# Kernel optimization log

Hardware: AMD Instinct MI355X
Metric: run time of the kernel (lower is better)

Reference implementation:

```python
import jax, jax.numpy as jnp
import numpy as np

B, S, D, H = 2, 2048, 1024, 16
DH = D // H  # dim per head (dim_singl_head)
SCALE = 0.02


def layer_norm(x, g, b, eps=1e-5):
    m = jnp.mean(x, axis=-1, keepdims=True)
    v = jnp.mean((x - m) ** 2, axis=-1, keepdims=True)
    return (x - m) / jnp.sqrt(v + eps) * g + b


def setup_inputs() -> dict:
    key = jax.random.key(0)
    ks = jax.random.split(key, 12)
    return {
        "query": jax.random.normal(ks[0], (B, S, D), jnp.float32),
        "key": jax.random.normal(ks[1], (B, S, D), jnp.float32),
        "value": jax.random.normal(ks[2], (B, S, D), jnp.float32),
        "mask": jax.random.randint(ks[3], (B, S), 0, 2).astype(jnp.int32),
        "Wq": jax.random.normal(ks[4], (D, D), jnp.float32) * SCALE,
        "bq": jnp.zeros((D,), jnp.float32),
        "Wk": jax.random.normal(ks[5], (D, D), jnp.float32) * SCALE,
        "bk": jnp.zeros((D,), jnp.float32),
        "Wv": jax.random.normal(ks[6], (D, D), jnp.float32) * SCALE,
        "bv": jnp.zeros((D,), jnp.float32),
        "g_att": jnp.ones((DH,), jnp.float32),
        "b_att": jnp.zeros((DH,), jnp.float32),
        "Wres": jax.random.normal(ks[7], (D, D), jnp.float32) * SCALE,
        "bres": jnp.zeros((D,), jnp.float32),
        "g_out": jnp.ones((D,), jnp.float32),
        "b_out": jnp.zeros((D,), jnp.float32),
    }


def reference(query, key, value, mask, Wq, bq, Wk, bk, Wv, bv,
              g_att, b_att, Wres, bres, g_out, b_out):
    # split heads: torch's split(dh,-1)+cat(dim=0) == [H,B,S,dh] layout
    def heads(x):
        return x.reshape(B, S, H, DH).transpose(2, 0, 1, 3)  # [H,B,S,dh]

    q = heads(query @ Wq + bq)
    k = heads(key @ Wk + bk)
    v = heads(value @ Wv + bv)

    # additive mask: (1-mask)*-1e9, broadcast [1,B,1,Sk]
    madd = (1.0 - mask.astype(q.dtype))[None, :, None, :] * -1e9

    scores = jnp.einsum('hbqd,hbkd->hbqk', q, k) / np.float32(np.sqrt(DH))
    w = jax.nn.softmax(scores + madd, axis=-1)
    out = jnp.einsum('hbqk,hbkd->hbqd', w, v)

    out = out + q                         # residual_att
    out = layer_norm(out, g_att, b_att)   # per-head LayerNorm on dh

    # concat heads back: [H,B,S,dh] -> [B,S,H*dh]
    out = out.transpose(1, 2, 0, 3).reshape(B, S, D)

    out = out + jnp.tanh(out @ Wres + bres)  # residual_out branch
    out = layer_norm(out, g_out, b_out)      # norm_out
    return jnp.tanh(out)                     # final activation
```

## Files before the change

kernel.cpp:

```cpp
#include <hip/hip_runtime.h>
#include <cstdint>
#include <cstddef>

#define BB 2
#define SS 2048
#define DD 1024
#define HH 16
#define DHH 64
#define MROWS (BB*SS)

typedef short short8 __attribute__((ext_vector_type(8)));
typedef short short4v __attribute__((ext_vector_type(4)));
typedef float floatx4 __attribute__((ext_vector_type(4)));

#define GAS __attribute__((address_space(1)))
#define LAS __attribute__((address_space(3)))

#if !defined(__HIP_DEVICE_COMPILE__)
#define MFMA16(a, b, c) (c)
#elif __has_builtin(__builtin_amdgcn_mfma_f32_16x16x16bf16_1k)
#define MFMA16(a, b, c) __builtin_amdgcn_mfma_f32_16x16x16bf16_1k((a), (b), (c), 0, 0, 0)
#elif __has_builtin(__builtin_amdgcn_mfma_f32_16x16x16_bf16)
#define MFMA16(a, b, c) __builtin_amdgcn_mfma_f32_16x16x16_bf16((a), (b), (c), 0, 0, 0)
#elif __has_builtin(__builtin_amdgcn_mfma_f32_16x16x16_bf16_1k)
#define MFMA16(a, b, c) __builtin_amdgcn_mfma_f32_16x16x16_bf16_1k((a), (b), (c), 0, 0, 0)
#else
#error "no 16x16x16 bf16 MFMA builtin found on device pass"
#endif

__device__ __forceinline__ float4 ld4(const float* p) { return *(const float4*)p; }

__device__ __forceinline__ short f2bf(float x) {
    unsigned u = __builtin_bit_cast(unsigned, x);
    unsigned r = (u + 0x7fffu + ((u >> 16) & 1u)) >> 16;
    return (short)r;
}

__device__ __forceinline__ void gl_lds16(const short* g, short* l) {
    __builtin_amdgcn_global_load_lds((const GAS unsigned int*)g,
                                     (LAS unsigned int*)l, 16, 0, 0);
}

__global__ __launch_bounds__(256) void transpose_w_kernel(
    const float* __restrict__ W0, const float* __restrict__ W1,
    const float* __restrict__ W2, const float* __restrict__ W3,
    short* __restrict__ T0, short* __restrict__ T1,
    short* __restrict__ T2, short* __restrict__ T3)
{
    const float* W; short* T;
    if (blockIdx.z == 0)      { W = W0; T = T0; }
    else if (blockIdx.z == 1) { W = W1; T = T1; }
    else if (blockIdx.z == 2) { W = W2; T = T2; }
    else                      { W = W3; T = T3; }

    __shared__ short tile[64 * 72];
    const int t  = threadIdx.x;
    const int k0 = blockIdx.x * 64, n0 = blockIdx.y * 64;
#pragma unroll
    for (int i = 0; i < 4; i++) {
        int flat = i * 256 + t;
        int row = flat >> 4;
        int c4  = (flat & 15) * 4;
        float4 v = ld4(W + (size_t)(k0 + row) * DD + n0 + c4);
        tile[(c4 + 0) * 72 + row] = f2bf(v.x);
        tile[(c4 + 1) * 72 + row] = f2bf(v.y);
        tile[(c4 + 2) * 72 + row] = f2bf(v.z);
        tile[(c4 + 3) * 72 + row] = f2bf(v.w);
    }
    __syncthreads();
#pragma unroll
    for (int i = 0; i < 4; i++) {
        int flat = i * 256 + t;
        int nrow = flat >> 4;
        int kc   = (flat & 15) * 4;
        short4v pk = *(short4v*)&tile[nrow * 72 + kc];
        *(short4v*)(T + (size_t)(n0 + nrow) * DD + k0 + kc) = pk;
    }
}

__global__ __launch_bounds__(256) void gemm_bf16_kernel(
    const float* __restrict__ A0, const float* __restrict__ A1, const float* __restrict__ A2,
    const short* __restrict__ Bt0, const short* __restrict__ Bt1, const short* __restrict__ Bt2,
    const float* __restrict__ b0, const float* __restrict__ b1, const float* __restrict__ b2,
    float* __restrict__ Cf0, float* __restrict__ Cf1, float* __restrict__ Cf2,
    short* __restrict__ Cb0, short* __restrict__ Cb1, short* __restrict__ Cb2,
    short* __restrict__ Ct0, short* __restrict__ Ct1, short* __restrict__ Ct2,
    float cs0, float cs1, float cs2)
{
    const float* A; const short* Bt; const float* bias;
    float* Cf; short* Cb; short* Ct; float cbs;
    if (blockIdx.z == 0)      { A = A0; Bt = Bt0; bias = b0; Cf = Cf0; Cb = Cb0; Ct = Ct0; cbs = cs0; }
    else if (blockIdx.z == 1) { A = A1; Bt = Bt1; bias = b1; Cf = Cf1; Cb = Cb1; Ct = Ct1; cbs = cs1; }
    else                      { A = A2; Bt = Bt2; bias = b2; Cf = Cf2; Cb = Cb2; Ct = Ct2; cbs = cs2; }

    __shared__ __align__(16) short As[2 * 128 * 32];
    __shared__ __align__(16) short Bs[2 * 128 * 32];

    const int tid  = threadIdx.x;
    const int lane = tid & 63;
    const int wave = tid >> 6;
    const int quad = lane >> 4;
    const int l15  = lane & 15;
    const int m0 = blockIdx.y * 128;
    const int n0 = blockIdx.x * 128;
    const int wr = (wave >> 1) * 64;
    const int wc = (wave & 1) * 64;

    const int arow = tid >> 2;
    const int ach  = tid & 3;

    floatx4 acc[4][4];
#pragma unroll
    for (int mt = 0; mt < 4; mt++)
#pragma unroll
        for (int nt = 0; nt < 4; nt++) acc[mt][nt] = (floatx4)0.0f;

    float4 fa[2][2];
#pragma unroll
    for (int i = 0; i < 2; i++) {
        int c = tid + i * 256;
        gl_lds16(Bt + (size_t)(n0 + (c >> 2)) * DD + (c & 3) * 8, &Bs[c * 8]);
    }
#pragma unroll
    for (int i = 0; i < 2; i++) {
        const float* ap = A + (size_t)(m0 + arow + i * 64) * DD + ach * 8;
        fa[i][0] = ld4(ap);
        fa[i][1] = ld4(ap + 4);
    }

    for (int kk = 0; kk < 32; kk++) {
        const int bufo = (kk & 1) * 4096;
#pragma unroll
        for (int i = 0; i < 2; i++) {
            short8 s8;
            s8[0] = f2bf(fa[i][0].x); s8[1] = f2bf(fa[i][0].y);
            s8[2] = f2bf(fa[i][0].z); s8[3] = f2bf(fa[i][0].w);
            s8[4] = f2bf(fa[i][1].x); s8[5] = f2bf(fa[i][1].y);
            s8[6] = f2bf(fa[i][1].z); s8[7] = f2bf(fa[i][1].w);
            *(short8*)&As[bufo + (arow + i * 64) * 32 + ach * 8] = s8;
        }
        __syncthreads();

        if (kk < 31) {
            const int k0n = (kk + 1) * 32;
            const int nbuf = bufo ^ 4096;
#pragma unroll
            for (int i = 0; i < 2; i++) {
                int c = tid + i * 256;
                gl_lds16(Bt + (size_t)(n0 + (c >> 2)) * DD + k0n + (c & 3) * 8,
                         &Bs[nbuf + c * 8]);
            }
#pragma unroll
            for (int i = 0; i < 2; i++) {
                const float* ap = A + (size_t)(m0 + arow + i * 64) * DD + k0n + ach * 8;
                fa[i][0] = ld4(ap);
                fa[i][1] = ld4(ap + 4);
            }
        }

        short8 af[4], bf[4];
#pragma unroll
        for (int mt = 0; mt < 4; mt++)
            af[mt] = *(const short8*)&As[bufo + (wr + mt * 16 + l15) * 32 + quad * 8];
#pragma unroll
        for (int nt = 0; nt < 4; nt++)
            bf[nt] = *(const short8*)&Bs[bufo + (wc + nt * 16 + l15) * 32 + quad * 8];
#pragma unroll
        for (int mt = 0; mt < 4; mt++)
#pragma unroll
            for (int nt = 0; nt < 4; nt++)
                acc[mt][nt] = __builtin_amdgcn_mfma_f32_16x16x32_bf16(af[mt], bf[nt], acc[mt][nt], 0, 0, 0);
    }

    float biasv[4];
#pragma unroll
    for (int nt = 0; nt < 4; nt++) biasv[nt] = bias[n0 + wc + nt * 16 + l15];

    if (Cf || Cb) {
#pragma unroll
        for (int mt = 0; mt < 4; mt++)
#pragma unroll
            for (int r = 0; r < 4; r++) {
                const int m = m0 + wr + mt * 16 + quad * 4 + r;
                const size_t rowb = (size_t)m * DD + n0 + wc;
#pragma unroll
                for (int nt = 0; nt < 4; nt++) {
                    float v = acc[mt][nt][r] + biasv[nt];
                    if (Cf) Cf[rowb + nt * 16 + l15] = v;
                    if (Cb) Cb[rowb + nt * 16 + l15] = f2bf(v * cbs);
                }
            }
    }
    if (Ct) {
#pragma unroll
        for (int mt = 0; mt < 4; mt++) {
            const int mbase = m0 + wr + mt * 16 + quad * 4;
            const int bb = mbase >> 11;
            const int s0 = mbase & 2047;
#pragma unroll
            for (int nt = 0; nt < 4; nt++) {
                const int c = n0 + wc + nt * 16 + l15;
                short4v pk;
#pragma unroll
                for (int r = 0; r < 4; r++) pk[r] = f2bf(acc[mt][nt][r] + biasv[nt]);
                *(short4v*)(Ct + ((size_t)(bb * 1024 + c)) * SS + s0) = pk;
            }
        }
    }
}

__global__ __launch_bounds__(256, 4) void attn_mfma_kernel(
    const short* __restrict__ Qb, const short* __restrict__ Kb, const short* __restrict__ Vt,
    const float* __restrict__ Qf, const int* __restrict__ mask,
    const float* __restrict__ g_att, const float* __restrict__ b_att,
    float* __restrict__ X)
{
    const int tid  = threadIdx.x;
    const int lane = tid & 63;
    const int wave = tid >> 6;
    const int quad = lane >> 4;
    const int l15  = lane & 15;

    const int h  = blockIdx.y;
    const int b  = blockIdx.z;
    const int q0 = blockIdx.x * 128;
    const int bS = b * SS;

    __shared__ __align__(16) short Ks[2 * 64 * 72];
    __shared__ __align__(16) short Vs[2 * 64 * 72];
    __shared__ __align__(16) float smv[2 * 64];

    short8 qf[2][2];
#pragma unroll
    for (int qt = 0; qt < 2; qt++)
#pragma unroll
        for (int s = 0; s < 2; s++)
            qf[qt][s] = *(const short8*)(Qb +
                (size_t)(bS + q0 + wave * 32 + qt * 16 + l15) * DD + h * 64 + s * 32 + quad * 8);

    floatx4 o[4][2];
#pragma unroll
    for (int dt = 0; dt < 4; dt++)
#pragma unroll
        for (int qt = 0; qt < 2; qt++) o[dt][qt] = (floatx4)0.0f;
    float lsum[2] = {0.0f, 0.0f};

    const int srow = tid >> 3;
    const int sch  = tid & 7;

    short8 kreg[2], vreg[2];
    float mreg;
#pragma unroll
    for (int i = 0; i < 2; i++) {
        int row = srow + i * 32;
        kreg[i] = *(const short8*)(Kb + (size_t)(bS + row) * DD + h * 64 + sch * 8);
        vreg[i] = *(const short8*)(Vt + (size_t)(b * 1024 + h * 64 + row) * SS + sch * 8);
    }
    mreg = (tid < 64) ? (float)mask[bS + tid] : 0.0f;

    for (int kt = 0; kt < SS / 64; kt++) {
        const int bufo = (kt & 1) * (64 * 72);
        const int mvo  = (kt & 1) * 64;
#pragma unroll
        for (int i = 0; i < 2; i++) {
            int row = srow + i * 32;
            *(short8*)&Ks[bufo + row * 72 + sch * 8] = kreg[i];
            *(short8*)&Vs[bufo + row * 72 + sch * 8] = vreg[i];
        }
        if (tid < 64) smv[mvo + tid] = mreg;

        if (kt < SS / 64 - 1) {
            const int k0n = (kt + 1) * 64;
#pragma unroll
            for (int i = 0; i < 2; i++) {
                int row = srow + i * 32;
                kreg[i] = *(const short8*)(Kb + (size_t)(bS + k0n + row) * DD + h * 64 + sch * 8);
                vreg[i] = *(const short8*)(Vt + (size_t)(b * 1024 + h * 64 + row) * SS + k0n + sch * 8);
            }
            mreg = (tid < 64) ? (float)mask[bS + k0n + tid] : 0.0f;
        }

        __builtin_amdgcn_s_waitcnt(0xC07F);
        __builtin_amdgcn_s_barrier();

        short4v pf[4][2];
#pragma unroll
        for (int kt4 = 0; kt4 < 4; kt4++) {
            short8 kf0 = *(const short8*)&Ks[bufo + (kt4 * 16 + l15) * 72 + quad * 8];
            short8 kf1 = *(const short8*)&Ks[bufo + (kt4 * 16 + l15) * 72 + 32 + quad * 8];
            floatx4 mv = *(const floatx4*)&smv[mvo + kt4 * 16 + quad * 4];
#pragma unroll
            for (int qt = 0; qt < 2; qt++) {
                floatx4 st = (floatx4)0.0f;
                st = __builtin_amdgcn_mfma_f32_16x16x32_bf16(kf0, qf[qt][0], st, 0, 0, 0);
                st = __builtin_amdgcn_mfma_f32_16x16x32_bf16(kf1, qf[qt][1], st, 0, 0, 0);
                short4v pk;
#pragma unroll
                for (int r = 0; r < 4; r++) {
                    float p = __expf(st[r]) * mv[r];
                    lsum[qt] += p;
                    pk[r] = f2bf(p);
                }
                pf[kt4][qt] = pk;
            }
        }

#pragma unroll
        for (int dt = 0; dt < 4; dt++)
#pragma unroll
            for (int ks = 0; ks < 4; ks++) {
                short4v vf = *(const short4v*)&Vs[bufo + (dt * 16 + l15) * 72 + ks * 16 + quad * 4];
#pragma unroll
                for (int qt = 0; qt < 2; qt++)
                    o[dt][qt] = MFMA16(vf, pf[ks][qt], o[dt][qt]);
            }
    }

#pragma unroll
    for (int qt = 0; qt < 2; qt++) {
        lsum[qt] += __shfl_xor(lsum[qt], 16);
        lsum[qt] += __shfl_xor(lsum[qt], 32);
    }

#pragma unroll
    for (int qt = 0; qt < 2; qt++) {
        const int q = q0 + wave * 32 + qt * 16 + l15;
        const size_t base = (size_t)(bS + q) * DD + h * 64;
        const float rl = 1.0f / lsum[qt];

        float x[4][4];
        float sum = 0.0f;
#pragma unroll
        for (int dt = 0; dt < 4; dt++) {
            float4 qr = ld4(Qf + base + dt * 16 + quad * 4);
            x[dt][0] = o[dt][qt][0] * rl + qr.x;
            x[dt][1] = o[dt][qt][1] * rl + qr.y;
            x[dt][2] = o[dt][qt][2] * rl + qr.z;
            x[dt][3] = o[dt][qt][3] * rl + qr.w;
            sum += x[dt][0] + x[dt][1] + x[dt][2] + x[dt][3];
        }
        sum += __shfl_xor(sum, 16);
        sum += __shfl_xor(sum, 32);
        const float mu = sum * (1.0f / 64.0f);

        float vs = 0.0f;
#pragma unroll
        for (int dt = 0; dt < 4; dt++)
#pragma unroll
            for (int r = 0; r < 4; r++) { float d = x[dt][r] - mu; vs += d * d; }
        vs += __shfl_xor(vs, 16);
        vs += __shfl_xor(vs, 32);
        const float rstd = rsqrtf(vs * (1.0f / 64.0f) + 1e-5f);

#pragma unroll
        for (int dt = 0; dt < 4; dt++) {
            float4 gv = ld4(g_att + dt * 16 + quad * 4);
            float4 bv = ld4(b_att + dt * 16 + quad * 4);
            float4 y;
            y.x = (x[dt][0] - mu) * rstd * gv.x + bv.x;
            y.y = (x[dt][1] - mu) * rstd * gv.y + bv.y;
            y.z = (x[dt][2] - mu) * rstd * gv.z + bv.z;
            y.w = (x[dt][3] - mu) * rstd * gv.w + bv.w;
            *(float4*)(X + base + dt * 16 + quad * 4) = y;
        }
    }
}

__global__ __launch_bounds__(256) void lnout_kernel(
    const float* __restrict__ X, const float* __restrict__ Y,
    const float* __restrict__ g, const float* __restrict__ bcoef,
    float* __restrict__ out)
{
    const int r = blockIdx.x;
    const int t = threadIdx.x;
    const size_t base = (size_t)r * DD + (t << 2);
    float4 x = ld4(X + base);
    float4 y = ld4(Y + base);
    float4 z;
    z.x = x.x + tanhf(y.x);
    z.y = x.y + tanhf(y.y);
    z.z = x.z + tanhf(y.z);
    z.w = x.w + tanhf(y.w);

    __shared__ float red[4];
    __shared__ float stats[2];
    const int w = t >> 6;

    float sv = z.x + z.y + z.z + z.w;
#pragma unroll
    for (int off = 32; off > 0; off >>= 1) sv += __shfl_down(sv, off);
    if ((t & 63) == 0) red[w] = sv;
    __syncthreads();
    if (t == 0) stats[0] = (red[0] + red[1] + red[2] + red[3]) * (1.0f / 1024.0f);
    __syncthreads();
    const float mu = stats[0];

    float4 d;
    d.x = z.x - mu; d.y = z.y - mu; d.z = z.z - mu; d.w = z.w - mu;
    float s2 = d.x * d.x + d.y * d.y + d.z * d.z + d.w * d.w;
#pragma unroll
    for (int off = 32; off > 0; off >>= 1) s2 += __shfl_down(s2, off);
    if ((t & 63) == 0) red[w] = s2;
    __syncthreads();
    if (t == 0) stats[1] = rsqrtf((red[0] + red[1] + red[2] + red[3]) * (1.0f / 1024.0f) + 1e-5f);
    __syncthreads();
    const float rstd = stats[1];

    float4 gv = ld4(g + (t << 2));
    float4 bv = ld4(bcoef + (t << 2));
    float4 o;
    o.x = tanhf(d.x * rstd * gv.x + bv.x);
    o.y = tanhf(d.y * rstd * gv.y + bv.y);
    o.z = tanhf(d.z * rstd * gv.z + bv.z);
    o.w = tanhf(d.w * rstd * gv.w + bv.w);
    *(float4*)(out + base) = o;
}

extern "C" void kernel_launch(void* const* d_in, const int* in_sizes, int n_in,
                              void* d_out, int out_size, void* d_ws, size_t ws_size,
                              hipStream_t stream)
{
    const float* query = (const float*)d_in[0];
    const float* key   = (const float*)d_in[1];
    const float* value = (const float*)d_in[2];
    const int*   mask  = (const int*)  d_in[3];
    const float* Wq    = (const float*)d_in[4];
    const float* bq    = (const float*)d_in[5];
    const float* Wk    = (const float*)d_in[6];
    const float* bk    = (const float*)d_in[7];
    const float* Wv    = (const float*)d_in[8];
    const float* bv    = (const float*)d_in[9];
    const float* g_att = (const float*)d_in[10];
    const float* b_att = (const float*)d_in[11];
    const float* Wres  = (const float*)d_in[12];
    const float* bres  = (const float*)d_in[13];
    const float* g_out = (const float*)d_in[14];
    const float* b_out = (const float*)d_in[15];

    const size_t MAT = (size_t)MROWS * DD;
    float* fws = (float*)d_ws;
    float* Qw = fws;
    float* Xw = fws + MAT;
    float* Yw = fws + 2 * MAT;
    short* Qb = (short*)(fws + 3 * MAT);
    short* Kb = Qb + MAT;
    short* Vt = Kb + MAT;
    short* Wtq = Vt + MAT;
    short* Wtk = Wtq + DD * DD;
    short* Wtv = Wtk + DD * DD;
    short* Wtr = Wtv + DD * DD;

    transpose_w_kernel<<<dim3(16, 16, 4), 256, 0, stream>>>(
        Wq, Wk, Wv, Wres, Wtq, Wtk, Wtv, Wtr);

    gemm_bf16_kernel<<<dim3(8, 32, 3), 256, 0, stream>>>(
        query, key, value, Wtq, Wtk, Wtv, bq, bk, bv,
        Qw, nullptr, nullptr,
        Qb, Kb, nullptr,
        nullptr, nullptr, Vt,
        0.125f, 1.0f, 1.0f);

    attn_mfma_kernel<<<dim3(SS / 128, HH, BB), 256, 0, stream>>>(
        Qb, Kb, Vt, Qw, mask, g_att, b_att, Xw);

    gemm_bf16_kernel<<<dim3(8, 32, 1), 256, 0, stream>>>(
        Xw, Xw, Xw, Wtr, Wtr, Wtr, bres, bres, bres,
        Yw, Yw, Yw, nullptr, nullptr, nullptr, nullptr, nullptr, nullptr,
        1.0f, 1.0f, 1.0f);

    lnout_kernel<<<MROWS, 256, 0, stream>>>(Xw, Yw, g_out, b_out, (float*)d_out);
}
```

Measured before the change: 309.9 us.

## Pre-convert activations to bf16, restructure GEMM loads and attention tiling

```diff
diff --git a/kernel.cpp b/kernel.cpp
--- a/kernel.cpp
+++ b/kernel.cpp
@@ -16,18 +16,6 @@
 #define GAS __attribute__((address_space(1)))
 #define LAS __attribute__((address_space(3)))
 
-#if !defined(__HIP_DEVICE_COMPILE__)
-#define MFMA16(a, b, c) (c)
-#elif __has_builtin(__builtin_amdgcn_mfma_f32_16x16x16bf16_1k)
-#define MFMA16(a, b, c) __builtin_amdgcn_mfma_f32_16x16x16bf16_1k((a), (b), (c), 0, 0, 0)
-#elif __has_builtin(__builtin_amdgcn_mfma_f32_16x16x16_bf16)
-#define MFMA16(a, b, c) __builtin_amdgcn_mfma_f32_16x16x16_bf16((a), (b), (c), 0, 0, 0)
-#elif __has_builtin(__builtin_amdgcn_mfma_f32_16x16x16_bf16_1k)
-#define MFMA16(a, b, c) __builtin_amdgcn_mfma_f32_16x16x16_bf16_1k((a), (b), (c), 0, 0, 0)
-#else
-#error "no 16x16x16 bf16 MFMA builtin found on device pass"
-#endif
-
 __device__ __forceinline__ float4 ld4(const float* p) { return *(const float4*)p; }
 
 __device__ __forceinline__ short f2bf(float x) {
@@ -39,6 +27,23 @@
 __device__ __forceinline__ void gl_lds16(const short* g, short* l) {
     __builtin_amdgcn_global_load_lds((const GAS unsigned int*)g,
                                      (LAS unsigned int*)l, 16, 0, 0);
+}
+
+__global__ __launch_bounds__(256) void convert_kernel(
+    const float* __restrict__ s0, const float* __restrict__ s1, const float* __restrict__ s2,
+    short* __restrict__ d0, short* __restrict__ d1, short* __restrict__ d2)
+{
+    const float* s; short* d;
+    if (blockIdx.z == 0)      { s = s0; d = d0; }
+    else if (blockIdx.z == 1) { s = s1; d = d1; }
+    else                      { s = s2; d = d2; }
+    size_t idx = ((size_t)blockIdx.x * 256 + threadIdx.x) * 8;
+    float4 a = ld4(s + idx);
+    float4 b = ld4(s + idx + 4);
+    short8 p;
+    p[0] = f2bf(a.x); p[1] = f2bf(a.y); p[2] = f2bf(a.z); p[3] = f2bf(a.w);
+    p[4] = f2bf(b.x); p[5] = f2bf(b.y); p[6] = f2bf(b.z); p[7] = f2bf(b.w);
+    *(short8*)(d + idx) = p;
 }
 
 __global__ __launch_bounds__(256) void transpose_w_kernel(
@@ -78,23 +83,51 @@
     }
 }
 
+__global__ __launch_bounds__(256) void transpose_v_kernel(
+    const short* __restrict__ Vb, short* __restrict__ Vt)
+{
+    __shared__ short tile[64 * 72];
+    const int t  = threadIdx.x;
+    const int sb = blockIdx.x * 64;
+    const int cb = blockIdx.y * 64;
+    const int b  = sb >> 11;
+    const int s0 = sb & 2047;
+#pragma unroll
+    for (int i = 0; i < 2; i++) {
+        int flat = i * 256 + t;
+        int r  = flat >> 3;
+        int ch = flat & 7;
+        short8 v = *(const short8*)(Vb + (size_t)(sb + r) * DD + cb + ch * 8);
+#pragma unroll
+        for (int j = 0; j < 8; j++) tile[(ch * 8 + j) * 72 + r] = v[j];
+    }
+    __syncthreads();
+#pragma unroll
+    for (int i = 0; i < 2; i++) {
+        int flat = i * 256 + t;
+        int cr = flat >> 3;
+        int sc = flat & 7;
+        short8 w = *(const short8*)&tile[cr * 72 + sc * 8];
+        *(short8*)(Vt + ((size_t)(b * 1024 + cb + cr)) * SS + s0 + sc * 8) = w;
+    }
+}
+
 __global__ __launch_bounds__(256) void gemm_bf16_kernel(
-    const float* __restrict__ A0, const float* __restrict__ A1, const float* __restrict__ A2,
+    const short* __restrict__ A0, const short* __restrict__ A1, const short* __restrict__ A2,
     const short* __restrict__ Bt0, const short* __restrict__ Bt1, const short* __restrict__ Bt2,
     const float* __restrict__ b0, const float* __restrict__ b1, const float* __restrict__ b2,
     float* __restrict__ Cf0, float* __restrict__ Cf1, float* __restrict__ Cf2,
     short* __restrict__ Cb0, short* __restrict__ Cb1, short* __restrict__ Cb2,
-    short* __restrict__ Ct0, short* __restrict__ Ct1, short* __restrict__ Ct2,
     float cs0, float cs1, float cs2)
 {
-    const float* A; const short* Bt; const float* bias;
-    float* Cf; short* Cb; short* Ct; float cbs;
-    if (blockIdx.z == 0)      { A = A0; Bt = Bt0; bias = b0; Cf = Cf0; Cb = Cb0; Ct = Ct0; cbs = cs0; }
-    else if (blockIdx.z == 1) { A = A1; Bt = Bt1; bias = b1; Cf = Cf1; Cb = Cb1; Ct = Ct1; cbs = cs1; }
-    else                      { A = A2; Bt = Bt2; bias = b2; Cf = Cf2; Cb = Cb2; Ct = Ct2; cbs = cs2; }
-
-    __shared__ __align__(16) short As[2 * 128 * 32];
-    __shared__ __align__(16) short Bs[2 * 128 * 32];
+    const short* A; const short* Bt; const float* bias;
+    float* Cf; short* Cb; float cbs;
+    if (blockIdx.z == 0)      { A = A0; Bt = Bt0; bias = b0; Cf = Cf0; Cb = Cb0; cbs = cs0; }
+    else if (blockIdx.z == 1) { A = A1; Bt = Bt1; bias = b1; Cf = Cf1; Cb = Cb1; cbs = cs1; }
+    else                      { A = A2; Bt = Bt2; bias = b2; Cf = Cf2; Cb = Cb2; cbs = cs2; }
+
+    __shared__ __align__(16) short As[128 * 32];
+    __shared__ __align__(16) short Bs[128 * 32];
 
     const int tid  = threadIdx.x;
     const int lane = tid & 63;
@@ -106,65 +139,31 @@
     const int wr = (wave >> 1) * 64;
     const int wc = (wave & 1) * 64;
 
-    const int arow = tid >> 2;
-    const int ach  = tid & 3;
-
     floatx4 acc[4][4];
 #pragma unroll
     for (int mt = 0; mt < 4; mt++)
 #pragma unroll
         for (int nt = 0; nt < 4; nt++) acc[mt][nt] = (floatx4)0.0f;
 
-    float4 fa[2][2];
-#pragma unroll
-    for (int i = 0; i < 2; i++) {
-        int c = tid + i * 256;
-        gl_lds16(Bt + (size_t)(n0 + (c >> 2)) * DD + (c & 3) * 8, &Bs[c * 8]);
-    }
-#pragma unroll
-    for (int i = 0; i < 2; i++) {
-        const float* ap = A + (size_t)(m0 + arow + i * 64) * DD + ach * 8;
-        fa[i][0] = ld4(ap);
-        fa[i][1] = ld4(ap + 4);
-    }
-
-    for (int kk = 0; kk < 32; kk++) {
-        const int bufo = (kk & 1) * 4096;
-#pragma unroll
-        for (int i = 0; i < 2; i++) {
-            short8 s8;
-            s8[0] = f2bf(fa[i][0].x); s8[1] = f2bf(fa[i][0].y);
-            s8[2] = f2bf(fa[i][0].z); s8[3] = f2bf(fa[i][0].w);
-            s8[4] = f2bf(fa[i][1].x); s8[5] = f2bf(fa[i][1].y);
-            s8[6] = f2bf(fa[i][1].z); s8[7] = f2bf(fa[i][1].w);
-            *(short8*)&As[bufo + (arow + i * 64) * 32 + ach * 8] = s8;
-        }
+    for (int k0 = 0; k0 < DD; k0 += 32) {
         __syncthreads();
-
-        if (kk < 31) {
-            const int k0n = (kk + 1) * 32;
-            const int nbuf = bufo ^ 4096;
-#pragma unroll
-            for (int i = 0; i < 2; i++) {
-                int c = tid + i * 256;
-                gl_lds16(Bt + (size_t)(n0 + (c >> 2)) * DD + k0n + (c & 3) * 8,
-                         &Bs[nbuf + c * 8]);
-            }
-#pragma unroll
-            for (int i = 0; i < 2; i++) {
-                const float* ap = A + (size_t)(m0 + arow + i * 64) * DD + k0n + ach * 8;
-                fa[i][0] = ld4(ap);
-                fa[i][1] = ld4(ap + 4);
-            }
-        }
+#pragma unroll
+        for (int j = 0; j < 2; j++) {
+            int chunk = j * 256 + tid;
+            int row = chunk >> 2;
+            int ch  = chunk & 3;
+            gl_lds16(A  + (size_t)(m0 + row) * DD + k0 + ch * 8, &As[chunk * 8]);
+            gl_lds16(Bt + (size_t)(n0 + row) * DD + k0 + ch * 8, &Bs[chunk * 8]);
+        }
+        __syncthreads();
 
         short8 af[4], bf[4];
 #pragma unroll
         for (int mt = 0; mt < 4; mt++)
-            af[mt] = *(const short8*)&As[bufo + (wr + mt * 16 + l15) * 32 + quad * 8];
+            af[mt] = *(const short8*)&As[(wr + mt * 16 + l15) * 32 + quad * 8];
 #pragma unroll
         for (int nt = 0; nt < 4; nt++)
-            bf[nt] = *(const short8*)&Bs[bufo + (wc + nt * 16 + l15) * 32 + quad * 8];
+            bf[nt] = *(const short8*)&Bs[(wc + nt * 16 + l15) * 32 + quad * 8];
 #pragma unroll
         for (int mt = 0; mt < 4; mt++)
 #pragma unroll
@@ -176,44 +175,26 @@
 #pragma unroll
     for (int nt = 0; nt < 4; nt++) biasv[nt] = bias[n0 + wc + nt * 16 + l15];
 
-    if (Cf || Cb) {
-#pragma unroll
-        for (int mt = 0; mt < 4; mt++)
-#pragma unroll
-            for (int r = 0; r < 4; r++) {
-                const int m = m0 + wr + mt * 16 + quad * 4 + r;
-                const size_t rowb = (size_t)m * DD + n0 + wc;
-#pragma unroll
-                for (int nt = 0; nt < 4; nt++) {
-                    float v = acc[mt][nt][r] + biasv[nt];
-                    if (Cf) Cf[rowb + nt * 16 + l15] = v;
-                    if (Cb) Cb[rowb + nt * 16 + l15] = f2bf(v * cbs);
-                }
+#pragma unroll
+    for (int mt = 0; mt < 4; mt++)
+#pragma unroll
+        for (int r = 0; r < 4; r++) {
+            const int m = m0 + wr + mt * 16 + quad * 4 + r;
+            const size_t rowb = (size_t)m * DD + n0 + wc;
+#pragma unroll
+            for (int nt = 0; nt < 4; nt++) {
+                float v = acc[mt][nt][r] + biasv[nt];
+                if (Cf) Cf[rowb + nt * 16 + l15] = v;
+                if (Cb) Cb[rowb + nt * 16 + l15] = f2bf(v * cbs);
             }
-    }
-    if (Ct) {
-#pragma unroll
-        for (int mt = 0; mt < 4; mt++) {
-            const int mbase = m0 + wr + mt * 16 + quad * 4;
-            const int bb = mbase >> 11;
-            const int s0 = mbase & 2047;
-#pragma unroll
-            for (int nt = 0; nt < 4; nt++) {
-                const int c = n0 + wc + nt * 16 + l15;
-                short4v pk;
-#pragma unroll
-                for (int r = 0; r < 4; r++) pk[r] = f2bf(acc[mt][nt][r] + biasv[nt]);
-                *(short4v*)(Ct + ((size_t)(bb * 1024 + c)) * SS + s0) = pk;
-            }
-        }
-    }
-}
-
-__global__ __launch_bounds__(256, 4) void attn_mfma_kernel(
+        }
+}
+
+__global__ __launch_bounds__(256, 2) void attn_mfma_kernel(
     const short* __restrict__ Qb, const short* __restrict__ Kb, const short* __restrict__ Vt,
     const float* __restrict__ Qf, const int* __restrict__ mask,
     const float* __restrict__ g_att, const float* __restrict__ b_att,
-    float* __restrict__ X)
+    float* __restrict__ X, short* __restrict__ Xb)
 {
     const int tid  = threadIdx.x;
     const int lane = tid & 63;
@@ -223,27 +204,31 @@
 
     const int h  = blockIdx.y;
     const int b  = blockIdx.z;
-    const int q0 = blockIdx.x * 128;
+    const int q0 = blockIdx.x * 256;
+    const int qw0 = q0 + wave * 64;
     const int bS = b * SS;
 
     __shared__ __align__(16) short Ks[2 * 64 * 72];
     __shared__ __align__(16) short Vs[2 * 64 * 72];
+    __shared__ __align__(16) short Ps[4 * 64 * 72];
     __shared__ __align__(16) float smv[2 * 64];
 
-    short8 qf[2][2];
-#pragma unroll
-    for (int qt = 0; qt < 2; qt++)
+    short* Pw = &Ps[wave * 64 * 72];
+
+    short8 qf[4][2];
+#pragma unroll
+    for (int qt = 0; qt < 4; qt++)
 #pragma unroll
         for (int s = 0; s < 2; s++)
             qf[qt][s] = *(const short8*)(Qb +
-                (size_t)(bS + q0 + wave * 32 + qt * 16 + l15) * DD + h * 64 + s * 32 + quad * 8);
-
-    floatx4 o[4][2];
+                (size_t)(bS + qw0 + qt * 16 + l15) * DD + h * 64 + s * 32 + quad * 8);
+
+    floatx4 o[4][4];
 #pragma unroll
     for (int dt = 0; dt < 4; dt++)
 #pragma unroll
-        for (int qt = 0; qt < 2; qt++) o[dt][qt] = (floatx4)0.0f;
-    float lsum[2] = {0.0f, 0.0f};
+        for (int qt = 0; qt < 4; qt++) o[dt][qt] = (floatx4)0.0f;
+    float lsum[4] = {0.0f, 0.0f, 0.0f, 0.0f};
 
     const int srow = tid >> 3;
     const int sch  = tid & 7;
@@ -283,14 +268,13 @@
         __builtin_amdgcn_s_waitcnt(0xC07F);
         __builtin_amdgcn_s_barrier();
 
-        short4v pf[4][2];
 #pragma unroll
         for (int kt4 = 0; kt4 < 4; kt4++) {
             short8 kf0 = *(const short8*)&Ks[bufo + (kt4 * 16 + l15) * 72 + quad * 8];
             short8 kf1 = *(const short8*)&Ks[bufo + (kt4 * 16 + l15) * 72 + 32 + quad * 8];
             floatx4 mv = *(const floatx4*)&smv[mvo + kt4 * 16 + quad * 4];
 #pragma unroll
-            for (int qt = 0; qt < 2; qt++) {
+            for (int qt = 0; qt < 4; qt++) {
                 floatx4 st = (floatx4)0.0f;
                 st = __builtin_amdgcn_mfma_f32_16x16x32_bf16(kf0, qf[qt][0], st, 0, 0, 0);
                 st = __builtin_amdgcn_mfma_f32_16x16x32_bf16(kf1, qf[qt][1], st, 0, 0, 0);
@@ -301,30 +285,35 @@
                     lsum[qt] += p;
                     pk[r] = f2bf(p);
                 }
-                pf[kt4][qt] = pk;
+                *(short4v*)&Pw[(qt * 16 + l15) * 72 + kt4 * 16 + quad * 4] = pk;
             }
         }
 
 #pragma unroll
-        for (int dt = 0; dt < 4; dt++)
-#pragma unroll
-            for (int ks = 0; ks < 4; ks++) {
-                short4v vf = *(const short4v*)&Vs[bufo + (dt * 16 + l15) * 72 + ks * 16 + quad * 4];
-#pragma unroll
-                for (int qt = 0; qt < 2; qt++)
-                    o[dt][qt] = MFMA16(vf, pf[ks][qt], o[dt][qt]);
+        for (int s = 0; s < 2; s++) {
+            short8 pb[4];
+#pragma unroll
+            for (int qt = 0; qt < 4; qt++)
+                pb[qt] = *(const short8*)&Pw[(qt * 16 + l15) * 72 + s * 32 + quad * 8];
+#pragma unroll
+            for (int dt = 0; dt < 4; dt++) {
+                short8 vf = *(const short8*)&Vs[bufo + (dt * 16 + l15) * 72 + s * 32 + quad * 8];
+#pragma unroll
+                for (int qt = 0; qt < 4; qt++)
+                    o[dt][qt] = __builtin_amdgcn_mfma_f32_16x16x32_bf16(vf, pb[qt], o[dt][qt], 0, 0, 0);
             }
-    }
-
-#pragma unroll
-    for (int qt = 0; qt < 2; qt++) {
+        }
+    }
+
+#pragma unroll
+    for (int qt = 0; qt < 4; qt++) {
         lsum[qt] += __shfl_xor(lsum[qt], 16);
         lsum[qt] += __shfl_xor(lsum[qt], 32);
     }
 
 #pragma unroll
-    for (int qt = 0; qt < 2; qt++) {
-        const int q = q0 + wave * 32 + qt * 16 + l15;
+    for (int qt = 0; qt < 4; qt++) {
+        const int q = qw0 + qt * 16 + l15;
         const size_t base = (size_t)(bS + q) * DD + h * 64;
         const float rl = 1.0f / lsum[qt];
 
@@ -362,6 +351,9 @@
             y.z = (x[dt][2] - mu) * rstd * gv.z + bv.z;
             y.w = (x[dt][3] - mu) * rstd * gv.w + bv.w;
             *(float4*)(X + base + dt * 16 + quad * 4) = y;
+            short4v yb;
+            yb[0] = f2bf(y.x); yb[1] = f2bf(y.y); yb[2] = f2bf(y.z); yb[3] = f2bf(y.w);
+            *(short4v*)(Xb + base + dt * 16 + quad * 4) = yb;
         }
     }
 }
@@ -441,31 +433,40 @@
     float* fws = (float*)d_ws;
     float* Qw = fws;
     float* Xw = fws + MAT;
-    float* Yw = fws + 2 * MAT;
-    short* Qb = (short*)(fws + 3 * MAT);
-    short* Kb = Qb + MAT;
-    short* Vt = Kb + MAT;
-    short* Wtq = Vt + MAT;
+    short* Qb  = (short*)(fws + 2 * MAT);
+    short* Kb  = Qb + MAT;
+    short* Vt  = Kb + MAT;
+    short* qbf = Vt + MAT;
+    short* kbf = qbf + MAT;
+    short* vbf = kbf + MAT;
+    short* Wtq = vbf + MAT;
     short* Wtk = Wtq + DD * DD;
     short* Wtv = Wtk + DD * DD;
     short* Wtr = Wtv + DD * DD;
+    short* Vb = (short*)Xw;
+    short* Xb = qbf;
+    float* Yw = (float*)kbf;
+
+    convert_kernel<<<dim3(MAT / 2048, 1, 3), 256, 0, stream>>>(
+        query, key, value, qbf, kbf, vbf);
 
     transpose_w_kernel<<<dim3(16, 16, 4), 256, 0, stream>>>(
         Wq, Wk, Wv, Wres, Wtq, Wtk, Wtv, Wtr);
 
     gemm_bf16_kernel<<<dim3(8, 32, 3), 256, 0, stream>>>(
-        query, key, value, Wtq, Wtk, Wtv, bq, bk, bv,
+        qbf, kbf, vbf, Wtq, Wtk, Wtv, bq, bk, bv,
         Qw, nullptr, nullptr,
-        Qb, Kb, nullptr,
-        nullptr, nullptr, Vt,
+        Qb, Kb, Vb,
         0.125f, 1.0f, 1.0f);
 
-    attn_mfma_kernel<<<dim3(SS / 128, HH, BB), 256, 0, stream>>>(
-        Qb, Kb, Vt, Qw, mask, g_att, b_att, Xw);
+    transpose_v_kernel<<<dim3(64, 16), 256, 0, stream>>>(Vb, Vt);
+
+    attn_mfma_kernel<<<dim3(SS / 256, HH, BB), 256, 0, stream>>>(
+        Qb, Kb, Vt, Qw, mask, g_att, b_att, Xw, Xb);
 
     gemm_bf16_kernel<<<dim3(8, 32, 1), 256, 0, stream>>>(
-        Xw, Xw, Xw, Wtr, Wtr, Wtr, bres, bres, bres,
-        Yw, Yw, Yw, nullptr, nullptr, nullptr, nullptr, nullptr, nullptr,
+        Xb, Xb, Xb, Wtr, Wtr, Wtr, bres, bres, bres,
+        Yw, Yw, Yw, nullptr, nullptr, nullptr,
         1.0f, 1.0f, 1.0f);
 
     lnout_kernel<<<MROWS, 256, 0, stream>>>(Xw, Yw, g_out, b_out, (float*)d_out);
```

Measured after the change: 290.3 us. 6.3% less time.
